# Performance work log

Measured on AMD Instinct MI355X. Metric: run time of the kernel, lower is better.

## Reference

```python
import jax, jax.numpy as jnp
import numpy as np

LATENT = 128
STEPS = 2


def _ln(x, scale, bias, eps=1e-6):
    mu = jnp.mean(x, axis=-1, keepdims=True)
    var = jnp.mean(jnp.square(x - mu), axis=-1, keepdims=True)
    return (x - mu) * jax.lax.rsqrt(var + eps) * scale + bias


def _mlp2(x, W0, b0, W1, b1):
    x = jax.nn.relu(x @ W0 + b0)
    return jax.nn.relu(x @ W1 + b1)


def setup_inputs() -> dict:
    key = jax.random.key(0)
    ks = iter(jax.random.split(key, 64))
    N, E, Dn, De, Dg, L, S = 50000, 500000, 64, 32, 16, LATENT, STEPS
    sc = 0.02
    d = {}
    d['node_feats'] = jax.random.normal(next(ks), (N, Dn), jnp.float32)
    d['edge_feats'] = jax.random.normal(next(ks), (E, De), jnp.float32)
    d['globals_'] = jax.random.normal(next(ks), (1, Dg), jnp.float32)
    d['senders'] = jax.random.randint(next(ks), (E,), 0, N, jnp.int32)
    d['receivers'] = jax.random.randint(next(ks), (E,), 0, N, jnp.int32)
    d['emb_node_W'] = jax.random.normal(next(ks), (Dn, L), jnp.float32) * sc
    d['emb_node_b'] = jnp.zeros((L,), jnp.float32)
    d['emb_edge_W'] = jax.random.normal(next(ks), (De, L), jnp.float32) * sc
    d['emb_edge_b'] = jnp.zeros((L,), jnp.float32)
    d['emb_glob_W'] = jax.random.normal(next(ks), (Dg, L), jnp.float32) * sc
    d['emb_glob_b'] = jnp.zeros((L,), jnp.float32)
    # per-step stacked params; edge/node MLP input = 4L, global MLP input = 3L
    d['edge_W0'] = jax.random.normal(next(ks), (S, 4 * L, L), jnp.float32) * sc
    d['edge_b0'] = jnp.zeros((S, L), jnp.float32)
    d['edge_W1'] = jax.random.normal(next(ks), (S, L, L), jnp.float32) * sc
    d['edge_b1'] = jnp.zeros((S, L), jnp.float32)
    d['node_W0'] = jax.random.normal(next(ks), (S, 4 * L, L), jnp.float32) * sc
    d['node_b0'] = jnp.zeros((S, L), jnp.float32)
    d['node_W1'] = jax.random.normal(next(ks), (S, L, L), jnp.float32) * sc
    d['node_b1'] = jnp.zeros((S, L), jnp.float32)
    d['glob_W0'] = jax.random.normal(next(ks), (S, 3 * L, L), jnp.float32) * sc
    d['glob_b0'] = jnp.zeros((S, L), jnp.float32)
    d['glob_W1'] = jax.random.normal(next(ks), (S, L, L), jnp.float32) * sc
    d['glob_b1'] = jnp.zeros((S, L), jnp.float32)
    d['ln_node_s'] = jnp.ones((S, L), jnp.float32)
    d['ln_node_b'] = jnp.zeros((S, L), jnp.float32)
    d['ln_edge_s'] = jnp.ones((S, L), jnp.float32)
    d['ln_edge_b'] = jnp.zeros((S, L), jnp.float32)
    d['ln_glob_s'] = jnp.ones((S, L), jnp.float32)
    d['ln_glob_b'] = jnp.zeros((S, L), jnp.float32)
    d['dec_W'] = jax.random.normal(next(ks), (L, L), jnp.float32) * sc
    d['dec_b'] = jnp.zeros((L,), jnp.float32)
    return d


def reference(node_feats, edge_feats, globals_, senders, receivers,
              emb_node_W, emb_node_b, emb_edge_W, emb_edge_b, emb_glob_W, emb_glob_b,
              edge_W0, edge_b0, edge_W1, edge_b1,
              node_W0, node_b0, node_W1, node_b1,
              glob_W0, glob_b0, glob_W1, glob_b1,
              ln_node_s, ln_node_b, ln_edge_s, ln_edge_b, ln_glob_s, ln_glob_b,
              dec_W, dec_b):
    N, E = node_feats.shape[0], edge_feats.shape[0]
    nodes = node_feats @ emb_node_W + emb_node_b          # [N, L]
    edges = edge_feats @ emb_edge_W + emb_edge_b          # [E, L]
    glob = globals_ @ emb_glob_W + emb_glob_b             # [1, L]
    for s in range(STEPS):
        # --- edge update: concat(edges, nodes[senders], nodes[receivers], global) ---
        ge = jnp.broadcast_to(glob, (E, glob.shape[-1]))
        edge_in = jnp.concatenate([edges, nodes[senders], nodes[receivers], ge], axis=-1)
        e_new = _mlp2(edge_in, edge_W0[s], edge_b0[s], edge_W1[s], edge_b1[s])
        # --- node update: concat(nodes, sum edges by sender, sum edges by receiver, global) ---
        sent = jax.ops.segment_sum(e_new, senders, num_segments=N)
        recv = jax.ops.segment_sum(e_new, receivers, num_segments=N)
        gn = jnp.broadcast_to(glob, (N, glob.shape[-1]))
        node_in = jnp.concatenate([nodes, sent, recv, gn], axis=-1)
        n_new = _mlp2(node_in, node_W0[s], node_b0[s], node_W1[s], node_b1[s])
        # --- global update: concat(sum nodes, sum edges, global) ---
        node_agg = jnp.sum(n_new, axis=0, keepdims=True)
        edge_agg = jnp.sum(e_new, axis=0, keepdims=True)
        glob_in = jnp.concatenate([node_agg, edge_agg, glob], axis=-1)
        g_new = _mlp2(glob_in, glob_W0[s], glob_b0[s], glob_W1[s], glob_b1[s])
        # skip connections + layer norm
        nodes = _ln(n_new + nodes, ln_node_s[s], ln_node_b[s])
        edges = _ln(e_new + edges, ln_edge_s[s], ln_edge_b[s])
        glob = _ln(g_new + glob, ln_glob_s[s], ln_glob_b[s])
    globals_out = glob @ dec_W + dec_b
    return nodes, edges, globals_out
```

## Files before the change

### kernel.cpp

```cpp
#include <hip/hip_runtime.h>

#define L 128
#define NSTEPS 2
#define SCAN_B 250

typedef __attribute__((ext_vector_type(8))) short short8;
typedef __attribute__((ext_vector_type(4))) float f32x4;

static __device__ __forceinline__ unsigned short f2bf(float f) {
  unsigned int u = __float_as_uint(f);
  u += 0x7FFFu + ((u >> 16) & 1u);
  return (unsigned short)(u >> 16);
}
static __device__ __forceinline__ unsigned short f2bf_trunc(float f) {
  return (unsigned short)(__float_as_uint(f) >> 16);
}
static __device__ __forceinline__ float bf2f(unsigned short h) {
  return __uint_as_float(((unsigned int)h) << 16);
}
static __device__ __forceinline__ float bfhi(unsigned u) {
  return __uint_as_float(u & 0xFFFF0000u);
}
static __device__ __forceinline__ float bflo(unsigned u) {
  return __uint_as_float(u << 16);
}
static __device__ __forceinline__ unsigned packf(float x) {
  unsigned short h = f2bf(x);
  unsigned short l = f2bf_trunc(x - bf2f(h));
  return ((unsigned)h << 16) | l;
}
static __device__ __forceinline__ float unpackf(unsigned p) {
  return bfhi(p) + bflo(p);
}

static __device__ __forceinline__ void unpack8_hi(const unsigned* __restrict__ p, short8& ah) {
  uint4 q0 = *(const uint4*)p;
  uint4 q1 = *(const uint4*)(p + 4);
  union U { unsigned u[4]; short8 s; } A;
  A.u[0] = __builtin_amdgcn_perm(q0.y, q0.x, 0x07060302u);
  A.u[1] = __builtin_amdgcn_perm(q0.w, q0.z, 0x07060302u);
  A.u[2] = __builtin_amdgcn_perm(q1.y, q1.x, 0x07060302u);
  A.u[3] = __builtin_amdgcn_perm(q1.w, q1.z, 0x07060302u);
  ah = A.s;
}

__global__ void conv_frag_kernel(const float* __restrict__ in, unsigned short* __restrict__ out,
                                 int S) {
  int id = blockIdx.x * 256 + threadIdx.x;
  int total = S * 12 * 8192;
  if (id >= total) return;
  int chunkid = id >> 13;
  int within = id & 8191;
  int s = chunkid / 12, ks = chunkid % 12;
  int hl = within >> 12;
  int rem = within & 4095;
  int fn = rem >> 9;
  int rem2 = rem & 511;
  int c = rem2 >> 5;
  int rem3 = rem2 & 31;
  int g = rem3 >> 3;
  int j = rem3 & 7;
  int k = ks * 32 + g * 8 + j;
  int n = fn * 16 + c;
  float x = in[(size_t)s * 512 * 128 + (size_t)k * 128 + n];
  unsigned short h = f2bf(x);
  out[id] = hl ? f2bf_trunc(x - bf2f(h)) : h;
}

__global__ void conv_split_kernel(const float* __restrict__ in,
                                  unsigned short* __restrict__ hi,
                                  unsigned short* __restrict__ lo,
                                  int Ksrc, int Kkeep, int S) {
  int id = blockIdx.x * 256 + threadIdx.x;
  int nk = 128 * Kkeep;
  int total = S * nk;
  if (id >= total) return;
  int s = id / nk;
  int rem = id - s * nk;
  int n = rem / Kkeep;
  int k = rem - n * Kkeep;
  float x = in[(size_t)s * Ksrc * 128 + (size_t)k * 128 + n];
  unsigned short h = f2bf(x);
  hi[id] = h;
  lo[id] = f2bf(x - bf2f(h));
}

template<int K>
__global__ __launch_bounds__(128, 4)
void embed_reg_kernel(const float* __restrict__ feats, const float* __restrict__ W,
                      const float* __restrict__ bias,
                      float* __restrict__ outf, unsigned* __restrict__ outp,
                      unsigned short* __restrict__ outh, int M) {
  int j = threadIdx.x;
  float w[K];
#pragma unroll
  for (int k = 0; k < K; ++k) w[k] = W[k * L + j];
  float bb = bias[j];
  int ng = (M + 3) >> 2;
  for (int gi = blockIdx.x; gi < ng; gi += gridDim.x) {
    int r0 = gi * 4;
    int r[4];
#pragma unroll
    for (int ri = 0; ri < 4; ++ri) r[ri] = min(r0 + ri, M - 1);
    float acc[4] = {bb, bb, bb, bb};
#pragma unroll
    for (int k4 = 0; k4 < K; k4 += 4) {
#pragma unroll
      for (int ri = 0; ri < 4; ++ri) {
        float4 f = *(const float4*)(feats + (size_t)r[ri] * K + k4);
        acc[ri] = fmaf(f.x, w[k4], acc[ri]);
        acc[ri] = fmaf(f.y, w[k4 + 1], acc[ri]);
        acc[ri] = fmaf(f.z, w[k4 + 2], acc[ri]);
        acc[ri] = fmaf(f.w, w[k4 + 3], acc[ri]);
      }
    }
#pragma unroll
    for (int ri = 0; ri < 4; ++ri) {
      size_t o = (size_t)r[ri] * L + j;
      if (outf) outf[o] = acc[ri];
      if (outp) outp[o] = packf(acc[ri]);
      if (outh) outh[o] = f2bf(acc[ri]);
    }
  }
}

__global__ void glob_embed_fold_kernel(const float* __restrict__ gin,
                                       const float* __restrict__ W, const float* __restrict__ bias,
                                       float* __restrict__ glob,
                                       const float* __restrict__ eWg, const float* __restrict__ eb0,
                                       float* __restrict__ b0e,
                                       const float* __restrict__ nWg, const float* __restrict__ nb0,
                                       float* __restrict__ b0n,
                                       float* __restrict__ node_agg, float* __restrict__ edge_agg) {
  __shared__ float gl[128];
  int j = threadIdx.x;
  float acc = bias[j];
  for (int k = 0; k < 16; ++k) acc += gin[k] * W[k * L + j];
  glob[j] = acc;
  gl[j] = acc;
  node_agg[j] = 0.f;
  edge_agg[j] = 0.f;
  __syncthreads();
  float ae = eb0[j], an = nb0[j];
  for (int k = 0; k < 128; ++k) {
    float g = gl[k];
    ae = fmaf(g, eWg[k * L + j], ae);
    an = fmaf(g, nWg[k * L + j], an);
  }
  b0e[j] = ae;
  b0n[j] = an;
}

__global__ void hist_kernel(const int* __restrict__ senders, const int* __restrict__ receivers,
                            int* __restrict__ cnt1, int* __restrict__ cnt2, int E) {
  int e = blockIdx.x * 256 + threadIdx.x;
  if (e >= E) return;
  atomicAdd(&cnt1[senders[e]], 1);
  atomicAdd(&cnt2[receivers[e]], 1);
}

__global__ void scan_sum_kernel(const int* __restrict__ cnt, int* __restrict__ part,
                                int n, int chunk) {
  __shared__ int red[256];
  int b = blockIdx.x, t = threadIdx.x;
  int lo = b * chunk, hi = min(lo + chunk, n);
  red[t] = (lo + t < hi) ? cnt[lo + t] : 0;
  __syncthreads();
  for (int o = 128; o > 0; o >>= 1) { if (t < o) red[t] += red[t + o]; __syncthreads(); }
  if (t == 0) part[b] = red[0];
}

__global__ void scan_part_kernel(int* __restrict__ part, int nb) {
  if (threadIdx.x == 0) {
    int run = 0;
    for (int i = 0; i < nb; ++i) { int v = part[i]; part[i] = run; run += v; }
  }
}

__global__ void scan_write_kernel(const int* __restrict__ cnt, const int* __restrict__ part,
                                  int* __restrict__ rp, int n, int chunk, int E) {
  __shared__ int buf[256];
  int b = blockIdx.x, t = threadIdx.x;
  int lo = b * chunk, hi = min(lo + chunk, n);
  buf[t] = (lo + t < hi) ? cnt[lo + t] : 0;
  __syncthreads();
  if (t == 0) {
    int run = part[b];
    for (int i = 0; i < hi - lo; ++i) { rp[lo + i] = run; run += buf[i]; }
  }
  if (b == gridDim.x - 1 && t == 0) rp[n] = E;
}

__global__ void fill_kernel(const int* __restrict__ senders, const int* __restrict__ receivers,
                            const int* __restrict__ rp1, const int* __restrict__ rp2,
                            int* __restrict__ cnt1, int* __restrict__ cnt2,
                            int* __restrict__ el1, int* __restrict__ el2, int E) {
  int e = blockIdx.x * 256 + threadIdx.x;
  if (e >= E) return;
  int s = senders[e];
  int p = atomicAdd(&cnt1[s], 1);
  el1[rp1[s] + p] = e;
  int r = receivers[e];
  int q = atomicAdd(&cnt2[r], 1);
  el2[rp2[r] + q] = e;
}

__global__ __launch_bounds__(256) void gather_kernel(
    const unsigned short* __restrict__ e16,
    const int* __restrict__ rp1, const int* __restrict__ el1,
    const int* __restrict__ rp2, const int* __restrict__ el2,
    unsigned short* __restrict__ sent_h, unsigned short* __restrict__ recv_h, int N) {
  int t = threadIdx.x;
  int v = blockIdx.x * 16 + (t >> 4);
  if (v >= N) return;
  int cols = (t & 15) * 8;
  float a1[8], a2[8];
#pragma unroll
  for (int i = 0; i < 8; ++i) { a1[i] = 0.f; a2[i] = 0.f; }
  int s1 = rp1[v], n1 = rp1[v + 1] - s1;
  int s2 = rp2[v], n2 = rp2[v + 1] - s2;
  int mx = max(n1, n2);
  for (int j = 0; j < mx; ++j) {
    if (j < n1) {
      uint4 u = *(const uint4*)(e16 + (size_t)el1[s1 + j] * L + cols);
      a1[0] += bflo(u.x); a1[1] += bfhi(u.x);
      a1[2] += bflo(u.y); a1[3] += bfhi(u.y);
      a1[4] += bflo(u.z); a1[5] += bfhi(u.z);
      a1[6] += bflo(u.w); a1[7] += bfhi(u.w);
    }
    if (j < n2) {
      uint4 u = *(const uint4*)(e16 + (size_t)el2[s2 + j] * L + cols);
      a2[0] += bflo(u.x); a2[1] += bfhi(u.x);
      a2[2] += bflo(u.y); a2[3] += bfhi(u.y);
      a2[4] += bflo(u.z); a2[5] += bfhi(u.z);
      a2[6] += bflo(u.w); a2[7] += bfhi(u.w);
    }
  }
  short8 o1, o2;
#pragma unroll
  for (int i = 0; i < 8; ++i) { o1[i] = (short)f2bf(a1[i]); o2[i] = (short)f2bf(a2[i]); }
  *(short8*)(sent_h + (size_t)v * L + cols) = o1;
  *(short8*)(recv_h + (size_t)v * L + cols) = o2;
}

template<int ROWS, bool EDGE_MODE>
__global__ __launch_bounds__(ROWS, 2)
void block_step_kernel(const float* __restrict__ xf,
                       const unsigned* __restrict__ xp,
                       const unsigned short* __restrict__ g1h,
                       const unsigned short* __restrict__ g2h,
                       const int* __restrict__ idx1, const int* __restrict__ idx2,
                       const unsigned short* __restrict__ W0c,
                       const float* __restrict__ b0eff,
                       const unsigned short* __restrict__ W1h,
                       const unsigned short* __restrict__ W1l,
                       const float* __restrict__ b1,
                       const float* __restrict__ ln_s, const float* __restrict__ ln_b,
                       float* __restrict__ agg,
                       unsigned short* __restrict__ e_out,
                       float* __restrict__ xf_out,
                       unsigned* __restrict__ xp_out,
                       unsigned short* __restrict__ xh_out,
                       int M) {
  static_assert(ROWS == 128, "pipeline assumes 128 threads");
  constexpr int WAVES = ROWS / 64;
  __shared__ __align__(16) unsigned short SL[16384];

  const int t = threadIdx.x;
  const int lane = t & 63;
  const int wg = t >> 6;
  const int c = lane & 15;
  const int g = lane >> 4;
  const int m0 = blockIdx.x * ROWS;
  const int valid = min(M - m0, ROWS);
  const int wbase = wg * 64;

  int rc4[4], j1[4], j2[4];
#pragma unroll
  for (int rf = 0; rf < 4; ++rf) {
    int rl = wbase + rf * 16 + c;
    int rc = min(rl, valid - 1);
    rc4[rf] = m0 + rc;
    if (EDGE_MODE) { j1[rf] = idx1[rc4[rf]]; j2[rf] = idx2[rc4[rf]]; }
    else           { j1[rf] = rc4[rf];       j2[rf] = rc4[rf]; }
  }

  const f32x4 z4 = {0.f, 0.f, 0.f, 0.f};
  f32x4 acc[4][8];
#pragma unroll
  for (int rf = 0; rf < 4; ++rf)
#pragma unroll
    for (int fn = 0; fn < 8; ++fn) acc[rf][fn] = z4;

  short8 wreg[8];
  auto loadW = [&](int ks) {
    const unsigned short* src = W0c + (size_t)ks * 8192 + t * 8;
#pragma unroll
    for (int i = 0; i < 8; ++i) wreg[i] = *(const short8*)(src + i * 1024);
  };
  auto writeW = [&](int buf) {
    unsigned short* dst = &SL[buf * 8192 + t * 8];
#pragma unroll
    for (int i = 0; i < 8; ++i) *(short8*)(dst + i * 1024) = wreg[i];
  };

  auto load_frag = [&](int ks, short8* a) {
    int seg = ks >> 2, kk = ks & 3;
    if (seg == 0) {
      if (EDGE_MODE) {
#pragma unroll
        for (int rf = 0; rf < 4; ++rf) {
          const float* bp = xf + (size_t)rc4[rf] * L + g * 8 + kk * 32;
          float4 v0 = *(const float4*)bp;
          float4 v1 = *(const float4*)(bp + 4);
          a[rf][0] = (short)f2bf(v0.x); a[rf][1] = (short)f2bf(v0.y);
          a[rf][2] = (short)f2bf(v0.z); a[rf][3] = (short)f2bf(v0.w);
          a[rf][4] = (short)f2bf(v1.x); a[rf][5] = (short)f2bf(v1.y);
          a[rf][6] = (short)f2bf(v1.z); a[rf][7] = (short)f2bf(v1.w);
        }
      } else {
#pragma unroll
        for (int rf = 0; rf < 4; ++rf)
          unpack8_hi(xp + (size_t)rc4[rf] * L + g * 8 + kk * 32, a[rf]);
      }
    } else {
      const unsigned short* src = (seg == 1) ? g1h : g2h;
      const int* rsel = (seg == 1) ? j1 : j2;
#pragma unroll
      for (int rf = 0; rf < 4; ++rf)
        a[rf] = *(const short8*)(src + (size_t)rsel[rf] * L + g * 8 + kk * 32);
    }
  };

  auto mfma_phase = [&](int buf, const short8* a) {
#pragma unroll
    for (int fn = 0; fn < 8; ++fn) {
      int off = buf * 8192 + fn * 512 + c * 32 + g * 8;
      short8 bh = *(const short8*)&SL[off];
      short8 bl = *(const short8*)&SL[off + 4096];
#pragma unroll
      for (int rf = 0; rf < 4; ++rf) {
        acc[rf][fn] = __builtin_amdgcn_mfma_f32_16x16x32_bf16(a[rf], bh, acc[rf][fn], 0, 0, 0);
        acc[rf][fn] = __builtin_amdgcn_mfma_f32_16x16x32_bf16(a[rf], bl, acc[rf][fn], 0, 0, 0);
      }
    }
  };

  {
    short8 aA[4], aB[4];
    loadW(0);
    load_frag(0, aA);
    writeW(0);
    loadW(1);
    __syncthreads();
#pragma unroll
    for (int ks = 0; ks < 12; ++ks) {
      short8* aCur = (ks & 1) ? aB : aA;
      short8* aNxt = (ks & 1) ? aA : aB;
      if (ks < 11) load_frag(ks + 1, aNxt);
      mfma_phase(ks & 1, aCur);
      if (ks < 11) {
        writeW((ks & 1) ^ 1);
        if (ks < 10) loadW(ks + 2);
      }
      __syncthreads();
    }
  }

  unsigned short* Hbf = SL;
#pragma unroll
  for (int fn = 0; fn < 8; ++fn) {
    int col = fn * 16 + c;
    float bb = b0eff[col];
    int unit = col >> 3;
#pragma unroll
    for (int rf = 0; rf < 4; ++rf) {
#pragma unroll
      for (int ri = 0; ri < 4; ++ri) {
        int rl = wbase + rf * 16 + g * 4 + ri;
        float x = fmaxf(acc[rf][fn][ri] + bb, 0.f);
        Hbf[rl * 128 + ((unit ^ (rl & 15)) << 3) + (col & 7)] = f2bf(x);
      }
    }
  }

  f32x4 acc2[4][8];
#pragma unroll
  for (int rf = 0; rf < 4; ++rf)
#pragma unroll
    for (int fn = 0; fn < 8; ++fn) acc2[rf][fn] = z4;
#pragma unroll
  for (int ks = 0; ks < 4; ++ks) {
    short8 ah[4];
#pragma unroll
    for (int rf = 0; rf < 4; ++rf) {
      int rl = wbase + rf * 16 + c;
      int unit = ks * 4 + g;
      ah[rf] = *(const short8*)&Hbf[rl * 128 + ((unit ^ (rl & 15)) << 3)];
    }
#pragma unroll
    for (int fn = 0; fn < 8; ++fn) {
      size_t wb = (size_t)(fn * 16 + c) * 128 + ks * 32 + g * 8;
      short8 bh = *(const short8*)(W1h + wb);
      short8 bl = *(const short8*)(W1l + wb);
#pragma unroll
      for (int rf = 0; rf < 4; ++rf) {
        acc2[rf][fn] = __builtin_amdgcn_mfma_f32_16x16x32_bf16(ah[rf], bh, acc2[rf][fn], 0, 0, 0);
        acc2[rf][fn] = __builtin_amdgcn_mfma_f32_16x16x32_bf16(ah[rf], bl, acc2[rf][fn], 0, 0, 0);
      }
    }
  }

  float colagg[8];
#pragma unroll
  for (int fn = 0; fn < 8; ++fn) colagg[fn] = 0.f;

#pragma unroll
  for (int rf = 0; rf < 4; ++rf) {
    const int rb = wbase + rf * 16 + g * 4;
    float sum[4] = {0.f, 0.f, 0.f, 0.f}, sq[4] = {0.f, 0.f, 0.f, 0.f};
    float xv[8][4];
#pragma unroll
    for (int fn = 0; fn < 8; ++fn) {
      int col = fn * 16 + c;
      float bb = b1[col];
#pragma unroll
      for (int ri = 0; ri < 4; ++ri) {
        int row = rb + ri;
        float e = fmaxf(acc2[rf][fn][ri] + bb, 0.f);
        if (row < valid) {
          if (EDGE_MODE) e_out[(size_t)(m0 + row) * L + col] = f2bf(e);
          colagg[fn] += e;
          float xprev;
          if (EDGE_MODE) xprev = xf[(size_t)(m0 + row) * L + col];
          else           xprev = unpackf(xp[(size_t)(m0 + row) * L + col]);
          float x = e + xprev;
          xv[fn][ri] = x;
          sum[ri] += x;
          sq[ri] += x * x;
        } else {
          xv[fn][ri] = 0.f;
        }
      }
    }
#pragma unroll
    for (int mask = 1; mask <= 8; mask <<= 1) {
#pragma unroll
      for (int ri = 0; ri < 4; ++ri) {
        sum[ri] += __shfl_xor(sum[ri], mask);
        sq[ri] += __shfl_xor(sq[ri], mask);
      }
    }
    float mu[4], rs[4];
#pragma unroll
    for (int ri = 0; ri < 4; ++ri) {
      mu[ri] = sum[ri] * (1.f / 128.f);
      float var = sq[ri] * (1.f / 128.f) - mu[ri] * mu[ri];
      rs[ri] = rsqrtf(var + 1e-6f);
    }
#pragma unroll
    for (int fn = 0; fn < 8; ++fn) {
      int col = fn * 16 + c;
      float lns = ln_s[col], lnb = ln_b[col];
#pragma unroll
      for (int ri = 0; ri < 4; ++ri) {
        int row = rb + ri;
        if (row < valid) {
          float y = (xv[fn][ri] - mu[ri]) * rs[ri] * lns + lnb;
          if (xf_out) xf_out[(size_t)(m0 + row) * L + col] = y;
          if (xp_out) xp_out[(size_t)(m0 + row) * L + col] = packf(y);
          if (xh_out) xh_out[(size_t)(m0 + row) * L + col] = f2bf(y);
        }
      }
    }
  }

#pragma unroll
  for (int mask = 16; mask <= 32; mask <<= 1)
#pragma unroll
    for (int fn = 0; fn < 8; ++fn) colagg[fn] += __shfl_xor(colagg[fn], mask);
  __syncthreads();
  float* F = (float*)SL;
  if (lane < 16) {
#pragma unroll
    for (int fn = 0; fn < 8; ++fn) F[wg * 128 + fn * 16 + lane] = colagg[fn];
  }
  __syncthreads();
  if (t < 128) {
    float s = 0.f;
#pragma unroll
    for (int w = 0; w < WAVES; ++w) s += F[w * 128 + t];
    atomicAdd(agg + t, s);
  }
}

__global__ void glob_step_kernel(float* __restrict__ glob,
                                 float* __restrict__ node_agg, float* __restrict__ edge_agg,
                                 const float* __restrict__ W0, const float* __restrict__ b0,
                                 const float* __restrict__ W1, const float* __restrict__ b1,
                                 const float* __restrict__ ln_s, const float* __restrict__ ln_b,
                                 const float* __restrict__ eWg, const float* __restrict__ eb0,
                                 float* __restrict__ b0e,
                                 const float* __restrict__ nWg, const float* __restrict__ nb0,
                                 float* __restrict__ b0n) {
  __shared__ float gin[384];
  __shared__ float h[128];
  __shared__ float red4[4];
  __shared__ float gl[128];
  int j = threadIdx.x;
  gin[j] = node_agg[j];
  gin[128 + j] = edge_agg[j];
  gin[256 + j] = glob[j];
  __syncthreads();
  node_agg[j] = 0.f;
  edge_agg[j] = 0.f;
  float a = b0[j];
  for (int k = 0; k < 384; ++k) a += gin[k] * W0[k * L + j];
  h[j] = fmaxf(a, 0.f);
  __syncthreads();
  float o = b1[j];
  for (int k = 0; k < 128; ++k) o += h[k] * W1[k * L + j];
  o = fmaxf(o, 0.f);
  float x = o + gin[256 + j];
  float sum = x, sq = x * x;
  for (int m = 1; m < 64; m <<= 1) { sum += __shfl_xor(sum, m); sq += __shfl_xor(sq, m); }
  if ((j & 63) == 0) { red4[(j >> 6) * 2] = sum; red4[(j >> 6) * 2 + 1] = sq; }
  __syncthreads();
  sum = red4[0] + red4[2]; sq = red4[1] + red4[3];
  float mu = sum * (1.f / 128.f);
  float var = sq * (1.f / 128.f) - mu * mu;
  float rsd = rsqrtf(var + 1e-6f);
  float gnew = (x - mu) * rsd * ln_s[j] + ln_b[j];
  glob[j] = gnew;
  gl[j] = gnew;
  __syncthreads();
  if (eWg) {
    float ae = eb0[j], an = nb0[j];
    for (int k = 0; k < 128; ++k) {
      float g = gl[k];
      ae = fmaf(g, eWg[k * L + j], ae);
      an = fmaf(g, nWg[k * L + j], an);
    }
    b0e[j] = ae;
    b0n[j] = an;
  }
}

__global__ void decode_kernel(const float* __restrict__ glob, const float* __restrict__ W,
                              const float* __restrict__ bias, float* __restrict__ out) {
  int j = threadIdx.x;
  float a = bias[j];
  for (int k = 0; k < 128; ++k) a += glob[k] * W[k * L + j];
  out[j] = a;
}

extern "C" void kernel_launch(void* const* d_in, const int* in_sizes, int n_in,
                              void* d_out, int out_size, void* d_ws, size_t ws_size,
                              hipStream_t stream) {
  const float* node_feats = (const float*)d_in[0];
  const float* edge_feats = (const float*)d_in[1];
  const float* globals_   = (const float*)d_in[2];
  const int*   senders    = (const int*)d_in[3];
  const int*   receivers  = (const int*)d_in[4];
  const float* emb_node_W = (const float*)d_in[5];
  const float* emb_node_b = (const float*)d_in[6];
  const float* emb_edge_W = (const float*)d_in[7];
  const float* emb_edge_b = (const float*)d_in[8];
  const float* emb_glob_W = (const float*)d_in[9];
  const float* emb_glob_b = (const float*)d_in[10];
  const float* edge_W0 = (const float*)d_in[11];
  const float* edge_b0 = (const float*)d_in[12];
  const float* edge_W1 = (const float*)d_in[13];
  const float* edge_b1 = (const float*)d_in[14];
  const float* node_W0 = (const float*)d_in[15];
  const float* node_b0 = (const float*)d_in[16];
  const float* node_W1 = (const float*)d_in[17];
  const float* node_b1 = (const float*)d_in[18];
  const float* glob_W0 = (const float*)d_in[19];
  const float* glob_b0 = (const float*)d_in[20];
  const float* glob_W1 = (const float*)d_in[21];
  const float* glob_b1 = (const float*)d_in[22];
  const float* ln_node_s = (const float*)d_in[23];
  const float* ln_node_b = (const float*)d_in[24];
  const float* ln_edge_s = (const float*)d_in[25];
  const float* ln_edge_b = (const float*)d_in[26];
  const float* ln_glob_s = (const float*)d_in[27];
  const float* ln_glob_b = (const float*)d_in[28];
  const float* dec_W = (const float*)d_in[29];
  const float* dec_b = (const float*)d_in[30];

  const int N = in_sizes[0] / 64;
  const int E = in_sizes[1] / 32;

  float* nodes = (float*)d_out;
  float* edges = nodes + (size_t)N * L;
  float* gout  = edges + (size_t)E * L;

  char* wp = (char*)d_ws;
  auto alloc = [&](size_t bytes) -> char* {
    char* p = wp;
    wp += (bytes + 255) & ~(size_t)255;
    return p;
  };
  float* glob = (float*)alloc(512);
  float* node_agg = (float*)alloc(512);
  float* edge_agg = (float*)alloc(512);
  float* b0e_eff = (float*)alloc(512);
  float* b0n_eff = (float*)alloc(512);
  unsigned short* eW0c = (unsigned short*)alloc((size_t)NSTEPS * 12 * 8192 * 2);
  unsigned short* nW0c = (unsigned short*)alloc((size_t)NSTEPS * 12 * 8192 * 2);
  unsigned short* eW1h = (unsigned short*)alloc((size_t)NSTEPS * 128 * 128 * 2);
  unsigned short* eW1l = (unsigned short*)alloc((size_t)NSTEPS * 128 * 128 * 2);
  unsigned short* nW1h = (unsigned short*)alloc((size_t)NSTEPS * 128 * 128 * 2);
  unsigned short* nW1l = (unsigned short*)alloc((size_t)NSTEPS * 128 * 128 * 2);
  unsigned* nodes_p = (unsigned*)alloc((size_t)N * L * 4);
  unsigned short* nodes_h = (unsigned short*)alloc((size_t)N * L * 2);
  unsigned short* sent_h  = (unsigned short*)alloc((size_t)N * L * 2);
  unsigned short* recv_h  = (unsigned short*)alloc((size_t)N * L * 2);
  int* rp1 = (int*)alloc((size_t)(N + 1) * 4);
  int* rp2 = (int*)alloc((size_t)(N + 1) * 4);
  int* cnt1 = (int*)alloc((size_t)N * 4);
  int* cnt2 = (int*)alloc((size_t)N * 4);
  int* el1 = (int*)alloc((size_t)E * 4);
  int* el2 = (int*)alloc((size_t)E * 4);
  int* part = (int*)alloc(SCAN_B * 4);
  unsigned short* e16 = (unsigned short*)alloc((size_t)E * L * 2);
  (void)ws_size;

  conv_frag_kernel<<<(NSTEPS * 12 * 8192 + 255) / 256, 256, 0, stream>>>(edge_W0, eW0c, NSTEPS);
  conv_frag_kernel<<<(NSTEPS * 12 * 8192 + 255) / 256, 256, 0, stream>>>(node_W0, nW0c, NSTEPS);
  conv_split_kernel<<<(NSTEPS * 128 * 128 + 255) / 256, 256, 0, stream>>>(edge_W1, eW1h, eW1l, 128, 128, NSTEPS);
  conv_split_kernel<<<(NSTEPS * 128 * 128 + 255) / 256, 256, 0, stream>>>(node_W1, nW1h, nW1l, 128, 128, NSTEPS);

  embed_reg_kernel<64><<<2048, 128, 0, stream>>>(node_feats, emb_node_W, emb_node_b,
                                                 nullptr, nodes_p, nodes_h, N);
  embed_reg_kernel<32><<<4096, 128, 0, stream>>>(edge_feats, emb_edge_W, emb_edge_b,
                                                 edges, nullptr, nullptr, E);
  glob_embed_fold_kernel<<<1, 128, 0, stream>>>(globals_, emb_glob_W, emb_glob_b, glob,
                                                edge_W0 + 384 * L, edge_b0, b0e_eff,
                                                node_W0 + 384 * L, node_b0, b0n_eff,
                                                node_agg, edge_agg);

  const int chunk = (N + SCAN_B - 1) / SCAN_B;
  hipMemsetAsync(cnt1, 0, (size_t)N * 4, stream);
  hipMemsetAsync(cnt2, 0, (size_t)N * 4, stream);
  hist_kernel<<<(E + 255) / 256, 256, 0, stream>>>(senders, receivers, cnt1, cnt2, E);
  scan_sum_kernel<<<SCAN_B, 256, 0, stream>>>(cnt1, part, N, chunk);
  scan_part_kernel<<<1, 64, 0, stream>>>(part, SCAN_B);
  scan_write_kernel<<<SCAN_B, 256, 0, stream>>>(cnt1, part, rp1, N, chunk, E);
  scan_sum_kernel<<<SCAN_B, 256, 0, stream>>>(cnt2, part, N, chunk);
  scan_part_kernel<<<1, 64, 0, stream>>>(part, SCAN_B);
  scan_write_kernel<<<SCAN_B, 256, 0, stream>>>(cnt2, part, rp2, N, chunk, E);
  hipMemsetAsync(cnt1, 0, (size_t)N * 4, stream);
  hipMemsetAsync(cnt2, 0, (size_t)N * 4, stream);
  fill_kernel<<<(E + 255) / 256, 256, 0, stream>>>(senders, receivers, rp1, rp2, cnt1, cnt2, el1, el2, E);

  const int egrid = (E + 127) / 128;
  const int ngrid = (N + 127) / 128;

  for (int s = 0; s < NSTEPS; ++s) {
    const bool last = (s == NSTEPS - 1);

    block_step_kernel<128, true><<<egrid, 128, 0, stream>>>(
        edges, nullptr, nodes_h, nodes_h, senders, receivers,
        eW0c + (size_t)s * 12 * 8192, b0e_eff,
        eW1h + (size_t)s * 128 * 128, eW1l + (size_t)s * 128 * 128, edge_b1 + s * L,
        ln_edge_s + s * L, ln_edge_b + s * L,
        edge_agg, e16, edges, nullptr, nullptr, E);

    gather_kernel<<<(N + 15) / 16, 256, 0, stream>>>(e16, rp1, el1, rp2, el2, sent_h, recv_h, N);

    block_step_kernel<128, false><<<ngrid, 128, 0, stream>>>(
        nullptr, nodes_p, sent_h, recv_h, nullptr, nullptr,
        nW0c + (size_t)s * 12 * 8192, b0n_eff,
        nW1h + (size_t)s * 128 * 128, nW1l + (size_t)s * 128 * 128, node_b1 + s * L,
        ln_node_s + s * L, ln_node_b + s * L,
        node_agg, nullptr, last ? nodes : nullptr, last ? nullptr : nodes_p,
        last ? nullptr : nodes_h, N);

    glob_step_kernel<<<1, 128, 0, stream>>>(
        glob, node_agg, edge_agg,
        glob_W0 + (size_t)s * 384 * L, glob_b0 + s * L,
        glob_W1 + (size_t)s * 128 * L, glob_b1 + s * L,
        ln_glob_s + s * L, ln_glob_b + s * L,
        last ? nullptr : (edge_W0 + (size_t)1 * 512 * L + 384 * L),
        last ? nullptr : (edge_b0 + 1 * L), b0e_eff,
        last ? nullptr : (node_W0 + (size_t)1 * 512 * L + 384 * L),
        last ? nullptr : (node_b0 + 1 * L), b0n_eff);
  }

  decode_kernel<<<1, 128, 0, stream>>>(glob, dec_W, dec_b, gout);
}
```

Baseline: 1.673 ms.

## Stream W0 chunks straight to LDS and deepen fragment prefetch

The W0 weight tiles now go straight from global memory into LDS with global_load_lds, replacing the register-staged load and LDS write. The A-fragment prefetch is deepened to three buffers, and hand-placed vmcnt waits with raw s_barrier replace __syncthreads. The fragment layout in the weight conversion kernel and the LDS read offsets are permuted to match the per-lane 16-byte direct-load layout. This removes VGPR pressure and the LDS write instructions from the main loop, but relies on exact vmcnt counting, which is fragile if the compiler reorders or merges loads.

```diff
diff --git a/kernel.cpp b/kernel.cpp
--- a/kernel.cpp
+++ b/kernel.cpp
@@ -56,9 +56,9 @@
   int rem = within & 4095;
   int fn = rem >> 9;
   int rem2 = rem & 511;
-  int c = rem2 >> 5;
-  int rem3 = rem2 & 31;
-  int g = rem3 >> 3;
+  int g = rem2 >> 7;
+  int rem3 = rem2 & 127;
+  int c = rem3 >> 3;
   int j = rem3 & 7;
   int k = ks * 32 + g * 8 + j;
   int n = fn * 16 + c;
@@ -242,6 +242,10 @@
   *(short8*)(sent_h + (size_t)v * L + cols) = o1;
   *(short8*)(recv_h + (size_t)v * L + cols) = o2;
 }
+
+#define WAITVM(n) do { __builtin_amdgcn_sched_barrier(0); \
+  asm volatile("s_waitcnt vmcnt(" #n ")"); \
+  __builtin_amdgcn_sched_barrier(0); } while (0)
 
 template<int ROWS, bool EDGE_MODE>
 __global__ __launch_bounds__(ROWS, 2)
@@ -292,16 +296,18 @@
 #pragma unroll
     for (int fn = 0; fn < 8; ++fn) acc[rf][fn] = z4;
 
-  short8 wreg[8];
-  auto loadW = [&](int ks) {
-    const unsigned short* src = W0c + (size_t)ks * 8192 + t * 8;
-#pragma unroll
-    for (int i = 0; i < 8; ++i) wreg[i] = *(const short8*)(src + i * 1024);
-  };
-  auto writeW = [&](int buf) {
-    unsigned short* dst = &SL[buf * 8192 + t * 8];
-#pragma unroll
-    for (int i = 0; i < 8; ++i) *(short8*)(dst + i * 1024) = wreg[i];
+  const char* wsrc = (const char*)W0c + (size_t)wg * 8192 + (size_t)lane * 16;
+  char* slbase = (char*)&SL[0] + (size_t)wg * 8192;
+  auto gllds_chunk = [&](int ks, int buf) {
+    const char* gb = wsrc + (size_t)ks * 16384;
+    char* lb = slbase + buf * 16384;
+#pragma unroll
+    for (int i = 0; i < 8; ++i) {
+      __builtin_amdgcn_global_load_lds(
+          (const __attribute__((address_space(1))) unsigned int*)(gb + i * 1024),
+          (__attribute__((address_space(3))) unsigned int*)(lb + i * 1024),
+          16, 0, 0);
+    }
   };
 
   auto load_frag = [&](int ks, short8* a) {
@@ -335,7 +341,7 @@
   auto mfma_phase = [&](int buf, const short8* a) {
 #pragma unroll
     for (int fn = 0; fn < 8; ++fn) {
-      int off = buf * 8192 + fn * 512 + c * 32 + g * 8;
+      int off = buf * 8192 + fn * 512 + g * 128 + c * 8;
       short8 bh = *(const short8*)&SL[off];
       short8 bl = *(const short8*)&SL[off + 4096];
 #pragma unroll
@@ -347,25 +353,29 @@
   };
 
   {
-    short8 aA[4], aB[4];
-    loadW(0);
-    load_frag(0, aA);
-    writeW(0);
-    loadW(1);
-    __syncthreads();
-#pragma unroll
-    for (int ks = 0; ks < 12; ++ks) {
-      short8* aCur = (ks & 1) ? aB : aA;
-      short8* aNxt = (ks & 1) ? aA : aB;
-      if (ks < 11) load_frag(ks + 1, aNxt);
-      mfma_phase(ks & 1, aCur);
-      if (ks < 11) {
-        writeW((ks & 1) ^ 1);
-        if (ks < 10) loadW(ks + 2);
-      }
-      __syncthreads();
-    }
-  }
+    short8 a[3][4];
+    gllds_chunk(0, 0);
+    load_frag(0, a[0]);
+    load_frag(1, a[1]);
+    WAITVM(8);
+    __builtin_amdgcn_s_barrier();
+
+#define STEP(ks, VMW)                                             \
+    {                                                             \
+      if ((ks) < 11) gllds_chunk((ks) + 1, ((ks) + 1) & 1);       \
+      if ((ks) < 10) load_frag((ks) + 2, a[((ks) + 2) % 3]);      \
+      mfma_phase((ks) & 1, a[(ks) % 3]);                          \
+      if ((ks) < 11) {                                            \
+        WAITVM(VMW);                                              \
+        __builtin_amdgcn_s_barrier();                             \
+      }                                                           \
+    }
+    STEP(0, 4) STEP(1, 4) STEP(2, 4) STEP(3, 4) STEP(4, 4)
+    STEP(5, 4) STEP(6, 4) STEP(7, 4) STEP(8, 4) STEP(9, 4)
+    STEP(10, 0) STEP(11, 0)
+#undef STEP
+  }
+  __syncthreads();
 
   unsigned short* Hbf = SL;
 #pragma unroll
```

After: 1.702 ms. No clear change (+1.7%).
